# Performance work log

Measured on AMD Instinct MI355X. Metric: run time of the kernel, lower is better.

## Reference

```python
import jax, jax.numpy as jnp
import numpy as np

N_NODES = 100000
N_EDGES = 3200000
F_IN = 64
F_OUT = 64
N_REL = 8


def setup_inputs() -> dict:
    key = jax.random.key(0)
    k1, k2, k3, k4, k5, k6 = jax.random.split(key, 6)
    x = jax.random.normal(k1, (N_NODES, F_IN), dtype=jnp.float32)
    edge_index = jax.random.randint(k2, (2, N_EDGES), 0, N_NODES, dtype=jnp.int64)
    edge_type = jax.random.randint(k3, (N_EDGES,), 0, N_REL, dtype=jnp.int64)
    # Glorot-ish init for relation weights, root weight, zero bias (PyG defaults)
    scale = 1.0 / np.sqrt(F_IN)
    weight = jax.random.normal(k4, (N_REL, F_IN, F_OUT), dtype=jnp.float32) * scale
    root = jax.random.normal(k5, (F_IN, F_OUT), dtype=jnp.float32) * scale
    bias = jnp.zeros((F_OUT,), dtype=jnp.float32)
    return {"x": x, "edge_index": edge_index, "edge_type": edge_type,
            "weight": weight, "root": root, "bias": bias}


def reference(x, edge_index, edge_type, weight, root, bias):
    """RGCNConv (PyG defaults: aggr='mean' per relation, root_weight, bias).

    out[i] = x[i] @ root + bias + sum_r mean_{j in N_r(i)} x[j] @ W[r]
    Since W[r] is linear, aggregate (segment-mean) first, transform after.
    """
    n_nodes = x.shape[0]
    n_rel = weight.shape[0]
    src, dst = edge_index[0], edge_index[1]
    xs = x[src]  # [E, F_IN] gathered source features (reused across relations)
    out = x @ root + bias  # [N, F_OUT]
    for r in range(n_rel):  # small fixed relation count
        mask = (edge_type == r).astype(x.dtype)  # [E]
        s = jax.ops.segment_sum(xs * mask[:, None], dst, num_segments=n_nodes)
        cnt = jax.ops.segment_sum(mask, dst, num_segments=n_nodes)
        agg = s / jnp.clip(cnt, 1.0)[:, None]  # per-relation mean over in-edges
        out = out + agg @ weight[r]
    return out
```

## Files before the change

kernel.cpp:

```cpp
#include <hip/hip_runtime.h>
#include <hip/hip_fp16.h>

#define NN 100000
#define NE 3200000
#define F 64
#define NR 8
#define NCB 98
#define CAPC 36864
#define CHUNKA 4000
#define NT 3125
#define SLCAP 1280

typedef _Float16 half8 __attribute__((ext_vector_type(8)));
typedef float f32x4 __attribute__((ext_vector_type(4)));
union U4H8 { uint4 u; half8 h; };

__global__ __launch_bounds__(128) void init_kernel(int* __restrict__ cursors) {
    int t = threadIdx.x;
    if (t < NCB) cursors[t] = t * CAPC;
}

__global__ __launch_bounds__(256) void cvt_kernel(
    const float* __restrict__ x, __half* __restrict__ xh)
{
    size_t base = ((size_t)blockIdx.x * 256 + threadIdx.x) * 8;
    float4 a = *(const float4*)(x + base);
    float4 b = *(const float4*)(x + base + 4);
    __half2 h0 = __floats2half2_rn(a.x, a.y);
    __half2 h1 = __floats2half2_rn(a.z, a.w);
    __half2 h2 = __floats2half2_rn(b.x, b.y);
    __half2 h3 = __floats2half2_rn(b.z, b.w);
    uint4 o;
    o.x = *(unsigned*)&h0; o.y = *(unsigned*)&h1;
    o.z = *(unsigned*)&h2; o.w = *(unsigned*)&h3;
    *(uint4*)(xh + base) = o;
}

__global__ __launch_bounds__(256) void cvtw_kernel(
    const float* __restrict__ weight, const float* __restrict__ root,
    __half* __restrict__ wt9)
{
    int gid = blockIdx.x * 256 + threadIdx.x;
    int s = gid >> 12;
    int rem = gid & 4095;
    int k = rem >> 6, n = rem & 63;
    const float* src = (s == 0) ? root : (weight + ((size_t)(s - 1) << 12));
    wt9[((size_t)s << 12) + (n << 6) + k] = __float2half_rn(src[(k << 6) + n]);
}

__global__ __launch_bounds__(256) void binA_kernel(
    const int* __restrict__ esrc, const int* __restrict__ edst,
    const int* __restrict__ etyp,
    int* __restrict__ cursors, unsigned* __restrict__ stag4)
{
    __shared__ int hist[128][4];
    __shared__ int start[128];
    __shared__ int cur[128][4];
    __shared__ int gbase[NCB];
    __shared__ unsigned recs[CHUNKA];
    __shared__ unsigned char bks[CHUNKA];

    const int t = threadIdx.x;
    const int cp = t & 3;
    const int e0 = blockIdx.x * CHUNKA;

    if (t < 128) ((int4*)hist)[t] = make_int4(0, 0, 0, 0);
    __syncthreads();

    unsigned pay[4][4];
    unsigned bk4[4];
    const uint4* sv4 = (const uint4*)(esrc + e0);
    const uint4* dv4 = (const uint4*)(edst + e0);
    const uint4* rv4 = (const uint4*)(etyp + e0);
#pragma unroll
    for (int j = 0; j < 4; j++) {
        int g = t + (j << 8);
        if (g < CHUNKA / 4) {
            uint4 sv = sv4[g];
            uint4 dv = dv4[g];
            uint4 rv = rv4[g];
            unsigned b0 = dv.x >> 10, b1 = dv.y >> 10, b2 = dv.z >> 10, b3 = dv.w >> 10;
            pay[j][0] = sv.x | ((dv.x & 1023u) << 17) | (rv.x << 27);
            pay[j][1] = sv.y | ((dv.y & 1023u) << 17) | (rv.y << 27);
            pay[j][2] = sv.z | ((dv.z & 1023u) << 17) | (rv.z << 27);
            pay[j][3] = sv.w | ((dv.w & 1023u) << 17) | (rv.w << 27);
            bk4[j] = b0 | (b1 << 8) | (b2 << 16) | (b3 << 24);
            atomicAdd(&hist[b0][cp], 1);
            atomicAdd(&hist[b1][cp], 1);
            atomicAdd(&hist[b2][cp], 1);
            atomicAdd(&hist[b3][cp], 1);
        }
    }
    __syncthreads();

    int tot = 0;
    if (t < 128) {
        int4 h4 = ((int4*)hist)[t];
        tot = h4.x + h4.y + h4.z + h4.w;
        start[t] = tot;
    }
    __syncthreads();
    for (int off = 1; off < 128; off <<= 1) {
        int v = 0;
        if (t < 128 && t >= off) v = start[t - off];
        __syncthreads();
        if (t < 128) start[t] += v;
        __syncthreads();
    }
    if (t < 128) start[t] -= tot;
    __syncthreads();
    if (t < NCB) {
        int4 h4 = ((int4*)hist)[t];
        int s = start[t];
        cur[t][0] = s;
        cur[t][1] = s + h4.x;
        cur[t][2] = s + h4.x + h4.y;
        cur[t][3] = s + h4.x + h4.y + h4.z;
        gbase[t] = atomicAdd(&cursors[t], tot);
    }
    __syncthreads();

#pragma unroll
    for (int j = 0; j < 4; j++) {
        int g = t + (j << 8);
        if (g < CHUNKA / 4) {
#pragma unroll
            for (int k = 0; k < 4; k++) {
                int b = (int)((bk4[j] >> (k << 3)) & 255u);
                int slot = atomicAdd(&cur[b][cp], 1);
                recs[slot] = pay[j][k];
                bks[slot] = (unsigned char)b;
            }
        }
    }
    __syncthreads();

#pragma unroll
    for (int j = 0; j < 16; j++) {
        int i = t + (j << 8);
        if (i < CHUNKA) {
            int b = (int)bks[i];
            stag4[gbase[b] + (i - start[b])] = recs[i];
        }
    }
}

__global__ __launch_bounds__(256) void binB_kernel(
    const unsigned* __restrict__ stag4, const int* __restrict__ cursors,
    unsigned* __restrict__ packed4, unsigned* __restrict__ runsd)
{
    __shared__ int h[32][4];
    __shared__ int cu[32][4];
    const int b = blockIdx.x >> 3;
    const int c = blockIdx.x & 7;
    const int t = threadIdx.x;
    const int cp = t & 3;
    const int bbase = b * CAPC;
    const int n = cursors[b] - bbase;
    const int s = (c == 0) ? 0 : (int)((((long long)c * n) >> 3) & ~3LL);
    const int e = (c == 7) ? n : (int)((((long long)(c + 1) * n) >> 3) & ~3LL);
    const int base = bbase + s;
    const int cn = e - s;

    if (t < 128) ((int*)h)[t] = 0;
    __syncthreads();

    unsigned pc[5][4];
    const uint4* src4 = (const uint4*)(stag4 + base);
#pragma unroll
    for (int j = 0; j < 5; j++) {
        int idx = (t + (j << 8)) << 2;
        if (idx < cn) {
            uint4 v = src4[t + (j << 8)];
            pc[j][0] = v.x; pc[j][1] = v.y; pc[j][2] = v.z; pc[j][3] = v.w;
#pragma unroll
            for (int k = 0; k < 4; k++)
                if (idx + k < cn) atomicAdd(&h[(pc[j][k] >> 22) & 31][cp], 1);
        }
    }
    __syncthreads();

    if (t < 32) {
        int h0 = h[t][0], h1 = h[t][1], h2 = h[t][2], h3 = h[t][3];
        int tot = h0 + h1 + h2 + h3;
        int v = tot;
#pragma unroll
        for (int off = 1; off < 32; off <<= 1) {
            int u = __shfl_up(v, off);
            if (t >= off) v += u;
        }
        int eb = v - tot;
        cu[t][0] = eb;
        cu[t][1] = eb + h0;
        cu[t][2] = eb + h0 + h1;
        cu[t][3] = eb + h0 + h1 + h2;
        runsd[(blockIdx.x << 5) + t] = ((unsigned)(base + eb) << 10) | (unsigned)tot;
    }
    __syncthreads();

#pragma unroll
    for (int j = 0; j < 5; j++) {
        int idx = (t + (j << 8)) << 2;
        if (idx < cn) {
#pragma unroll
            for (int k = 0; k < 4; k++) {
                if (idx + k < cn) {
                    unsigned v = pc[j][k];
                    unsigned f = (v >> 22) & 31u;
                    int p = atomicAdd(&cu[f][cp], 1);
                    unsigned d5  = (v >> 17) & 31u;
                    unsigned rel = v >> 27;
                    packed4[base + p] = (v & 0x1FFFFu) | (d5 << 17) | (rel << 22);
                }
            }
        }
    }
}

__global__ __launch_bounds__(128, 4) void fused_kernel(
    const __half* __restrict__ xh,
    const unsigned* __restrict__ packed4,
    const unsigned* __restrict__ runsd,
    const __half* __restrict__ wt9,
    const float* __restrict__ bias,
    float* __restrict__ out)
{
    __shared__ __align__(16) char Asb[32 * 128];
    __shared__ __align__(16) char Wtb[64 * 128];
    __shared__ int kstart[257];
    __shared__ int slist[SLCAP];
    __shared__ unsigned rdesc[8];
    __shared__ int wsum[2];
    int* const kcur = (int*)Asb;

    const int t = threadIdx.x;
    const int tile = blockIdx.x;
    const int lane = t & 63;
    const int wid = t >> 6;

    if (t < 8) rdesc[t] = runsd[(((tile >> 5) * 8 + t) << 5) + (tile & 31)];
    kstart[t] = 0; kstart[t + 128] = 0;
    __syncthreads();

    unsigned pc[8];
#pragma unroll
    for (int c = 0; c < 8; c++) {
        unsigned d = rdesc[c];
        int rs = (int)(d >> 10), rc = (int)(d & 1023u);
        if (t < rc) {
            pc[c] = packed4[rs + t];
            atomicAdd(&kstart[pc[c] >> 17], 1);
        }
        for (int i = t + 128; i < rc; i += 128)
            atomicAdd(&kstart[packed4[rs + i] >> 17], 1);
    }
    __syncthreads();

    const int a0 = kstart[2 * t], a1 = kstart[2 * t + 1];
    int v = a0 + a1;
#pragma unroll
    for (int off = 1; off < 64; off <<= 1) {
        int u = __shfl_up(v, off);
        if (lane >= off) v += u;
    }
    if (lane == 63) wsum[wid] = v;
    __syncthreads();
    const int wo = wid ? wsum[0] : 0;
    const int incl = wo + v;
    const int ebase = incl - a0 - a1;
    kstart[2 * t]     = ebase;
    kstart[2 * t + 1] = ebase + a0;
    kcur[2 * t]       = ebase;
    kcur[2 * t + 1]   = ebase + a0;
    if (t == 127) kstart[256] = incl;
    __syncthreads();

#pragma unroll
    for (int c = 0; c < 8; c++) {
        unsigned d = rdesc[c];
        int rs = (int)(d >> 10), rc = (int)(d & 1023u);
        if (t < rc) {
            int slot = atomicAdd(&kcur[pc[c] >> 17], 1);
            slist[slot] = (int)(pc[c] & 0x1FFFFu);
        }
        for (int i = t + 128; i < rc; i += 128) {
            unsigned p = packed4[rs + i];
            int slot = atomicAdd(&kcur[p >> 17], 1);
            slist[slot] = (int)(p & 0x1FFFFu);
        }
    }
    __syncthreads();

    const int node0 = tile * 32;
    const int w16 = wid << 4;
    const int sn  = w16 + (lane >> 2);
    const int sq  = lane & 3;
    const int kb  = sq << 3;
    const unsigned snswz = (unsigned)((sn & 7) << 4);
    char* const awp = Asb + sn * 128;

    const int ml = lane & 15;
    const int kg = lane >> 4;
    const int arow = w16 + ml;
    const unsigned aswz = (unsigned)((arow & 7) << 4);
    const unsigned kb0 = (unsigned)(kg << 4);

    f32x4 acc[4];
#pragma unroll
    for (int nt = 0; nt < 4; nt++)
#pragma unroll
        for (int i = 0; i < 4; i++) acc[nt][i] = 0.f;

    for (int seg = 0; seg < 9; seg++) {
        if (seg) __syncthreads();

        {
            const uint4* __restrict__ wsrc = (const uint4*)(wt9 + ((size_t)seg << 12));
#pragma unroll
            for (int j = 0; j < 4; j++) {
                int c = t + (j << 7);
                int n = c >> 3;
                unsigned kbyt = (unsigned)((c & 7) << 4);
                *(uint4*)(Wtb + n * 128 + (kbyt ^ (unsigned)((n & 7) << 4))) = wsrc[c];
            }
        }

        if (seg == 0) {
            const __half* rowp = xh + (size_t)(node0 + sn) * F + kb;
            uint4 va = *(const uint4*)(rowp);
            uint4 vb = *(const uint4*)(rowp + 32);
            *(uint4*)(awp + (((unsigned)(sq << 4)) ^ snswz)) = va;
            *(uint4*)(awp + ((64u | (unsigned)(sq << 4)) ^ snswz)) = vb;
        } else {
            const int key = ((seg - 1) << 5) | sn;
            const int beg = kstart[key];
            const int end = kstart[key + 1];
            float4 A0 = make_float4(0.f, 0.f, 0.f, 0.f);
            float4 A1 = A0, B0 = A0, B1 = A0;
            int i = beg;
            for (; i + 4 <= end; i += 4) {
                const __half* h0 = xh + (size_t)slist[i]     * F + kb;
                const __half* h1 = xh + (size_t)slist[i + 1] * F + kb;
                const __half* h2 = xh + (size_t)slist[i + 2] * F + kb;
                const __half* h3 = xh + (size_t)slist[i + 3] * F + kb;
                uint4 la0 = *(const uint4*)(h0);      uint4 lb0 = *(const uint4*)(h0 + 32);
                uint4 la1 = *(const uint4*)(h1);      uint4 lb1 = *(const uint4*)(h1 + 32);
                uint4 la2 = *(const uint4*)(h2);      uint4 lb2 = *(const uint4*)(h2 + 32);
                uint4 la3 = *(const uint4*)(h3);      uint4 lb3 = *(const uint4*)(h3 + 32);
#define ACC8(v, P, Q) { \
                float2 t0 = __half22float2(*(const __half2*)&(v).x); \
                float2 t1 = __half22float2(*(const __half2*)&(v).y); \
                float2 t2 = __half22float2(*(const __half2*)&(v).z); \
                float2 t3 = __half22float2(*(const __half2*)&(v).w); \
                P.x += t0.x; P.y += t0.y; P.z += t1.x; P.w += t1.y; \
                Q.x += t2.x; Q.y += t2.y; Q.z += t3.x; Q.w += t3.y; }
                ACC8(la0, A0, A1) ACC8(la1, A0, A1) ACC8(la2, A0, A1) ACC8(la3, A0, A1)
                ACC8(lb0, B0, B1) ACC8(lb1, B0, B1) ACC8(lb2, B0, B1) ACC8(lb3, B0, B1)
            }
            for (; i < end; i++) {
                const __half* h0 = xh + (size_t)slist[i] * F + kb;
                uint4 la = *(const uint4*)(h0);
                uint4 lb = *(const uint4*)(h0 + 32);
                ACC8(la, A0, A1)
                ACC8(lb, B0, B1)
            }
#undef ACC8
            const float scl = 1.0f / (float)max(end - beg, 1);
            __half2 p0 = __floats2half2_rn(A0.x * scl, A0.y * scl);
            __half2 p1 = __floats2half2_rn(A0.z * scl, A0.w * scl);
            __half2 p2 = __floats2half2_rn(A1.x * scl, A1.y * scl);
            __half2 p3 = __floats2half2_rn(A1.z * scl, A1.w * scl);
            __half2 q0 = __floats2half2_rn(B0.x * scl, B0.y * scl);
            __half2 q1 = __floats2half2_rn(B0.z * scl, B0.w * scl);
            __half2 q2 = __floats2half2_rn(B1.x * scl, B1.y * scl);
            __half2 q3 = __floats2half2_rn(B1.z * scl, B1.w * scl);
            uint4 pa, pb;
            pa.x = *(unsigned*)&p0; pa.y = *(unsigned*)&p1;
            pa.z = *(unsigned*)&p2; pa.w = *(unsigned*)&p3;
            pb.x = *(unsigned*)&q0; pb.y = *(unsigned*)&q1;
            pb.z = *(unsigned*)&q2; pb.w = *(unsigned*)&q3;
            *(uint4*)(awp + (((unsigned)(sq << 4)) ^ snswz)) = pa;
            *(uint4*)(awp + ((64u | (unsigned)(sq << 4)) ^ snswz)) = pb;
        }
        __syncthreads();

        U4H8 fa0, fa1;
        fa0.u = *(const uint4*)(Asb + arow * 128 + (kb0 ^ aswz));
        fa1.u = *(const uint4*)(Asb + arow * 128 + ((64u | kb0) ^ aswz));
#pragma unroll
        for (int nt = 0; nt < 4; nt++) {
            int wrow = (nt << 4) + ml;
            unsigned wswz = (unsigned)((wrow & 7) << 4);
            U4H8 fb0, fb1;
            fb0.u = *(const uint4*)(Wtb + wrow * 128 + (kb0 ^ wswz));
            fb1.u = *(const uint4*)(Wtb + wrow * 128 + ((64u | kb0) ^ wswz));
            acc[nt] = __builtin_amdgcn_mfma_f32_16x16x32_f16(fa0.h, fb0.h, acc[nt], 0, 0, 0);
            acc[nt] = __builtin_amdgcn_mfma_f32_16x16x32_f16(fa1.h, fb1.h, acc[nt], 0, 0, 0);
        }
    }

#pragma unroll
    for (int nt = 0; nt < 4; nt++) {
        float bb = bias[(nt << 4) + ml];
#pragma unroll
        for (int i = 0; i < 4; i++) {
            int node = node0 + w16 + (kg << 2) + i;
            out[(size_t)node * F + (nt << 4) + ml] = acc[nt][i] + bb;
        }
    }
}

extern "C" void kernel_launch(void* const* d_in, const int* in_sizes, int n_in,
                              void* d_out, int out_size, void* d_ws, size_t ws_size,
                              hipStream_t stream) {
    const float* x    = (const float*)d_in[0];
    const int*   ei   = (const int*)d_in[1];
    const int*   et   = (const int*)d_in[2];
    const float* wgt  = (const float*)d_in[3];
    const float* root = (const float*)d_in[4];
    const float* bias = (const float*)d_in[5];
    float*       out  = (float*)d_out;

    int*      cursors = (int*)d_ws;
    unsigned* runsd   = (unsigned*)((char*)d_ws + 512);
    unsigned* stag4   = (unsigned*)((char*)d_ws + 512 + 100352);
    unsigned* packed4 = stag4 + (size_t)NCB * CAPC;
    __half*   xh      = (__half*)(packed4 + (size_t)NCB * CAPC);
    __half*   wt9     = xh + (size_t)NN * F;

    init_kernel<<<1, 128, 0, stream>>>(cursors);
    cvt_kernel<<<NN * F / (256 * 8), 256, 0, stream>>>(x, xh);
    cvtw_kernel<<<144, 256, 0, stream>>>(wgt, root, wt9);
    binA_kernel<<<NE / CHUNKA, 256, 0, stream>>>(ei, ei + NE, et, cursors, stag4);
    binB_kernel<<<NCB * 8, 256, 0, stream>>>(stag4, cursors, packed4, runsd);
    fused_kernel<<<NT, 128, 0, stream>>>(xh, packed4, runsd, wt9, bias, out);
}
```

Baseline: 227.6 us.

## Drop second binning pass and filter bucket edges inside fused kernel

Removes the binB kernel and its packed4/run-descriptor buffers. Each fused tile now scans its whole coarse bucket from the staging buffer twice, keeps only edges whose sub-bucket field matches the tile, and builds its per-(relation, node) edge list directly in shared memory. This saves one kernel launch and the global write and re-read of the repacked edge array. In exchange, each of the 32 tiles in a bucket re-reads the full bucket from cache twice, which multiplies read traffic and per-thread filtering work. It also adds an SLCAP bound check on the shared list.

```diff
diff --git a/kernel.cpp b/kernel.cpp
--- a/kernel.cpp
+++ b/kernel.cpp
@@ -8,7 +8,7 @@
 #define NCB 98
 #define CAPC 36864
 #define CHUNKA 4000
-#define NT 3125
+#define NTI 3125
 #define SLCAP 1280
 
 typedef _Float16 half8 __attribute__((ext_vector_type(8)));
@@ -145,82 +145,10 @@
     }
 }
 
-__global__ __launch_bounds__(256) void binB_kernel(
-    const unsigned* __restrict__ stag4, const int* __restrict__ cursors,
-    unsigned* __restrict__ packed4, unsigned* __restrict__ runsd)
-{
-    __shared__ int h[32][4];
-    __shared__ int cu[32][4];
-    const int b = blockIdx.x >> 3;
-    const int c = blockIdx.x & 7;
-    const int t = threadIdx.x;
-    const int cp = t & 3;
-    const int bbase = b * CAPC;
-    const int n = cursors[b] - bbase;
-    const int s = (c == 0) ? 0 : (int)((((long long)c * n) >> 3) & ~3LL);
-    const int e = (c == 7) ? n : (int)((((long long)(c + 1) * n) >> 3) & ~3LL);
-    const int base = bbase + s;
-    const int cn = e - s;
-
-    if (t < 128) ((int*)h)[t] = 0;
-    __syncthreads();
-
-    unsigned pc[5][4];
-    const uint4* src4 = (const uint4*)(stag4 + base);
-#pragma unroll
-    for (int j = 0; j < 5; j++) {
-        int idx = (t + (j << 8)) << 2;
-        if (idx < cn) {
-            uint4 v = src4[t + (j << 8)];
-            pc[j][0] = v.x; pc[j][1] = v.y; pc[j][2] = v.z; pc[j][3] = v.w;
-#pragma unroll
-            for (int k = 0; k < 4; k++)
-                if (idx + k < cn) atomicAdd(&h[(pc[j][k] >> 22) & 31][cp], 1);
-        }
-    }
-    __syncthreads();
-
-    if (t < 32) {
-        int h0 = h[t][0], h1 = h[t][1], h2 = h[t][2], h3 = h[t][3];
-        int tot = h0 + h1 + h2 + h3;
-        int v = tot;
-#pragma unroll
-        for (int off = 1; off < 32; off <<= 1) {
-            int u = __shfl_up(v, off);
-            if (t >= off) v += u;
-        }
-        int eb = v - tot;
-        cu[t][0] = eb;
-        cu[t][1] = eb + h0;
-        cu[t][2] = eb + h0 + h1;
-        cu[t][3] = eb + h0 + h1 + h2;
-        runsd[(blockIdx.x << 5) + t] = ((unsigned)(base + eb) << 10) | (unsigned)tot;
-    }
-    __syncthreads();
-
-#pragma unroll
-    for (int j = 0; j < 5; j++) {
-        int idx = (t + (j << 8)) << 2;
-        if (idx < cn) {
-#pragma unroll
-            for (int k = 0; k < 4; k++) {
-                if (idx + k < cn) {
-                    unsigned v = pc[j][k];
-                    unsigned f = (v >> 22) & 31u;
-                    int p = atomicAdd(&cu[f][cp], 1);
-                    unsigned d5  = (v >> 17) & 31u;
-                    unsigned rel = v >> 27;
-                    packed4[base + p] = (v & 0x1FFFFu) | (d5 << 17) | (rel << 22);
-                }
-            }
-        }
-    }
-}
-
 __global__ __launch_bounds__(128, 4) void fused_kernel(
     const __half* __restrict__ xh,
-    const unsigned* __restrict__ packed4,
-    const unsigned* __restrict__ runsd,
+    const unsigned* __restrict__ stag4,
+    const int* __restrict__ cursors,
     const __half* __restrict__ wt9,
     const float* __restrict__ bias,
     float* __restrict__ out)
@@ -229,7 +157,6 @@
     __shared__ __align__(16) char Wtb[64 * 128];
     __shared__ int kstart[257];
     __shared__ int slist[SLCAP];
-    __shared__ unsigned rdesc[8];
     __shared__ int wsum[2];
     int* const kcur = (int*)Asb;
 
@@ -238,21 +165,29 @@
     const int lane = t & 63;
     const int wid = t >> 6;
 
-    if (t < 8) rdesc[t] = runsd[(((tile >> 5) * 8 + t) << 5) + (tile & 31)];
+    const int bkt  = tile >> 5;
+    const unsigned sub = (unsigned)(tile & 31);
+    const int bbase = bkt * CAPC;
+    const int n = cursors[bkt] - bbase;
+    const int n4 = n >> 2;
+
     kstart[t] = 0; kstart[t + 128] = 0;
     __syncthreads();
 
-    unsigned pc[8];
-#pragma unroll
-    for (int c = 0; c < 8; c++) {
-        unsigned d = rdesc[c];
-        int rs = (int)(d >> 10), rc = (int)(d & 1023u);
-        if (t < rc) {
-            pc[c] = packed4[rs + t];
-            atomicAdd(&kstart[pc[c] >> 17], 1);
-        }
-        for (int i = t + 128; i < rc; i += 128)
-            atomicAdd(&kstart[packed4[rs + i] >> 17], 1);
+#define KEY8(p) (int)((((p) >> 27) << 5) | (((p) >> 17) & 31u))
+    {
+        const uint4* s4 = (const uint4*)(stag4 + bbase);
+        for (int g = t; g < n4; g += 128) {
+            uint4 p = s4[g];
+            if (((p.x >> 22) & 31u) == sub) atomicAdd(&kstart[KEY8(p.x)], 1);
+            if (((p.y >> 22) & 31u) == sub) atomicAdd(&kstart[KEY8(p.y)], 1);
+            if (((p.z >> 22) & 31u) == sub) atomicAdd(&kstart[KEY8(p.z)], 1);
+            if (((p.w >> 22) & 31u) == sub) atomicAdd(&kstart[KEY8(p.w)], 1);
+        }
+        for (int i = (n4 << 2) + t; i < n; i += 128) {
+            unsigned p = stag4[bbase + i];
+            if (((p >> 22) & 31u) == sub) atomicAdd(&kstart[KEY8(p)], 1);
+        }
     }
     __syncthreads();
 
@@ -275,21 +210,23 @@
     if (t == 127) kstart[256] = incl;
     __syncthreads();
 
-#pragma unroll
-    for (int c = 0; c < 8; c++) {
-        unsigned d = rdesc[c];
-        int rs = (int)(d >> 10), rc = (int)(d & 1023u);
-        if (t < rc) {
-            int slot = atomicAdd(&kcur[pc[c] >> 17], 1);
-            slist[slot] = (int)(pc[c] & 0x1FFFFu);
-        }
-        for (int i = t + 128; i < rc; i += 128) {
-            unsigned p = packed4[rs + i];
-            int slot = atomicAdd(&kcur[p >> 17], 1);
-            slist[slot] = (int)(p & 0x1FFFFu);
-        }
-    }
-    __syncthreads();
+    {
+        const uint4* s4 = (const uint4*)(stag4 + bbase);
+        for (int g = t; g < n4; g += 128) {
+            uint4 p = s4[g];
+#define PUTE(P) if ((((P) >> 22) & 31u) == sub) { \
+            int slot = atomicAdd(&kcur[KEY8(P)], 1); \
+            if (slot < SLCAP) slist[slot] = (int)((P) & 0x1FFFFu); }
+            PUTE(p.x) PUTE(p.y) PUTE(p.z) PUTE(p.w)
+        }
+        for (int i = (n4 << 2) + t; i < n; i += 128) {
+            unsigned p = stag4[bbase + i];
+            PUTE(p)
+#undef PUTE
+        }
+    }
+    __syncthreads();
+#undef KEY8
 
     const int node0 = tile * 32;
     const int w16 = wid << 4;
@@ -319,9 +256,9 @@
 #pragma unroll
             for (int j = 0; j < 4; j++) {
                 int c = t + (j << 7);
-                int n = c >> 3;
+                int n2 = c >> 3;
                 unsigned kbyt = (unsigned)((c & 7) << 4);
-                *(uint4*)(Wtb + n * 128 + (kbyt ^ (unsigned)((n & 7) << 4))) = wsrc[c];
+                *(uint4*)(Wtb + n2 * 128 + (kbyt ^ (unsigned)((n2 & 7) << 4))) = wsrc[c];
             }
         }
 
@@ -421,17 +358,15 @@
     const float* bias = (const float*)d_in[5];
     float*       out  = (float*)d_out;
 
-    int*      cursors = (int*)d_ws;
-    unsigned* runsd   = (unsigned*)((char*)d_ws + 512);
-    unsigned* stag4   = (unsigned*)((char*)d_ws + 512 + 100352);
-    unsigned* packed4 = stag4 + (size_t)NCB * CAPC;
-    __half*   xh      = (__half*)(packed4 + (size_t)NCB * CAPC);
+    char* ws = (char*)d_ws;
+    int*      cursors = (int*)ws;
+    unsigned* stag4   = (unsigned*)(ws + 512);
+    __half*   xh      = (__half*)(stag4 + (size_t)NCB * CAPC);
     __half*   wt9     = xh + (size_t)NN * F;
 
     init_kernel<<<1, 128, 0, stream>>>(cursors);
     cvt_kernel<<<NN * F / (256 * 8), 256, 0, stream>>>(x, xh);
     cvtw_kernel<<<144, 256, 0, stream>>>(wgt, root, wt9);
     binA_kernel<<<NE / CHUNKA, 256, 0, stream>>>(ei, ei + NE, et, cursors, stag4);
-    binB_kernel<<<NCB * 8, 256, 0, stream>>>(stag4, cursors, packed4, runsd);
-    fused_kernel<<<NT, 128, 0, stream>>>(xh, packed4, runsd, wt9, bias, out);
-}
+    fused_kernel<<<NTI, 128, 0, stream>>>(xh, stag4, cursors, wt9, bias, out);
+}
```

New measurement: 323.8 us. 42.2% more time.
